# Kernel tuning notes

Hardware: AMD Instinct MI355X
Metric: run time of the kernel (lower is better)

The kernel has to match this reference:

```python
import jax, jax.numpy as jnp
import numpy as np

NUM_CP = 32

def setup_inputs() -> dict:
    key = jax.random.key(0)
    kx, kc = jax.random.split(key)
    x = jax.random.normal(kx, (64, 1048576), dtype=jnp.float32)
    control_points = jax.random.normal(kc, (NUM_CP,), dtype=jnp.float32) / np.sqrt(NUM_CP).astype(np.float32)
    knots = jnp.linspace(0.0, 1.0, NUM_CP, dtype=jnp.float32)
    return {"x": x, "control_points": control_points, "knots": knots}

def reference(x, control_points, knots):
    # normalize x to [0, ~1) exactly like the torch module
    xn = (x - x.min()) / (x.max() - x.min() + 1e-6)
    n = knots.shape[0]
    # bucketize: bin index i such that knots[i] <= xn < knots[i+1]
    # (points exactly on an interior knot give t=0 in the right bin, which equals
    idx = jnp.clip(jnp.searchsorted(knots, xn, side='right') - 1, 0, n - 2)
    k0 = knots[idx]
    k1 = knots[idx + 1]
    t = (xn - k0) / (k1 - k0)
    out = (1.0 - t) * control_points[idx] + t * control_points[idx + 1]
    # torch loop leaves points outside [knots[0], knots[-1]] at zero
    in_range = (xn >= knots[0]) & (xn <= knots[-1])
    return jnp.where(in_range, out, jnp.zeros((), dtype=out.dtype))
```

## Files before the change

### kernel.cpp

```cpp
#include <hip/hip_runtime.h>

typedef unsigned int u32;
typedef float vf4 __attribute__((ext_vector_type(4)));

__device__ __forceinline__ void nt_store4(float4* p, float4 v) {
    __builtin_nontemporal_store(*reinterpret_cast<vf4*>(&v), reinterpret_cast<vf4*>(p));
}
__device__ __forceinline__ float4 nt_load4(const float4* p) {
    vf4 t = __builtin_nontemporal_load(reinterpret_cast<const vf4*>(p));
    float4 r; r.x = t.x; r.y = t.y; r.z = t.z; r.w = t.w;
    return r;
}

__device__ __forceinline__ u32 f2ord(float f) {
    u32 b = __float_as_uint(f);
    return (b & 0x80000000u) ? ~b : (b | 0x80000000u);
}
__device__ __forceinline__ float ord2f(u32 k) {
    u32 b = (k & 0x80000000u) ? (k ^ 0x80000000u) : ~k;
    return __uint_as_float(b);
}

__global__ __launch_bounds__(256) void minmax_kernel(const float4* __restrict__ x, int n4,
                                                     u32* __restrict__ ws) {
    float mn = INFINITY, mx = -INFINITY;
    int stride = gridDim.x * blockDim.x;
    for (int i = blockIdx.x * blockDim.x + threadIdx.x; i < n4; i += stride) {
        float4 v = x[i];
        mn = fminf(mn, fminf(fminf(v.x, v.y), fminf(v.z, v.w)));
        mx = fmaxf(mx, fmaxf(fmaxf(v.x, v.y), fmaxf(v.z, v.w)));
    }
    #pragma unroll
    for (int off = 32; off > 0; off >>= 1) {
        mn = fminf(mn, __shfl_down(mn, off, 64));
        mx = fmaxf(mx, __shfl_down(mx, off, 64));
    }
    __shared__ float smn[4], smx[4];
    int wave = threadIdx.x >> 6;
    int lane = threadIdx.x & 63;
    if (lane == 0) { smn[wave] = mn; smx[wave] = mx; }
    __syncthreads();
    if (threadIdx.x == 0) {
        #pragma unroll
        for (int w = 1; w < 4; ++w) { mn = fminf(mn, smn[w]); mx = fmaxf(mx, smx[w]); }
        atomicMax(&ws[0], ~f2ord(mn));
        atomicMax(&ws[1],  f2ord(mx));
    }
}

__global__ __launch_bounds__(256) void apply_kernel(const float4* __restrict__ x,
                                                    const float* __restrict__ cp,
                                                    const float* __restrict__ knots,
                                                    const u32* __restrict__ ws,
                                                    float4* __restrict__ out, int n4) {
    __shared__ float sk[32];
    __shared__ float sa[32];
    __shared__ float sb[32];
    if (threadIdx.x < 32) {
        sk[threadIdx.x] = knots[threadIdx.x];
        sa[threadIdx.x] = cp[threadIdx.x];
    }
    __syncthreads();
    if (threadIdx.x < 31) {
        int i = threadIdx.x;
        sb[i] = (sa[i + 1] - sa[i]) / (sk[i + 1] - sk[i]);
    }
    __syncthreads();

    float mn = ord2f(~ws[0]);
    float mx = ord2f(ws[1]);
    float scale = 1.0f / (mx - mn + 1e-6f);
    float klo = sk[0], khi = sk[31];

    const int gtid   = blockIdx.x * blockDim.x + threadIdx.x;
    const int stride = gridDim.x * blockDim.x;
    const int KMAX   = (n4 + stride - 1) / stride;

    for (int k = KMAX - 1; k >= 0; --k) {
        const int i = k * stride + gtid;
        if (i >= n4) continue;
        float4 v = nt_load4(&x[i]);
        float4 r;
        float* vp = (float*)&v;
        float* rp = (float*)&r;
        #pragma unroll
        for (int c = 0; c < 4; ++c) {
            float xn = (vp[c] - mn) * scale;
            int b = (int)(xn * 31.0f);
            b = b < 0 ? 0 : (b > 30 ? 30 : b);
            if (xn < sk[b]) {
                b = (b > 0) ? b - 1 : 0;
            } else if (xn >= sk[b + 1]) {
                b = (b < 30) ? b + 1 : 30;
            }
            float val = fmaf(xn - sk[b], sb[b], sa[b]);
            rp[c] = (xn >= klo && xn <= khi) ? val : 0.0f;
        }
        nt_store4(&out[i], r);
    }
}

extern "C" void kernel_launch(void* const* d_in, const int* in_sizes, int n_in,
                              void* d_out, int out_size, void* d_ws, size_t ws_size,
                              hipStream_t stream) {
    const float* x     = (const float*)d_in[0];
    const float* cp    = (const float*)d_in[1];
    const float* knots = (const float*)d_in[2];
    float* out = (float*)d_out;
    u32* ws = (u32*)d_ws;

    int n  = in_sizes[0];
    int n4 = n / 4;

    hipMemsetAsync(ws, 0x00, 8, stream);

    minmax_kernel<<<4096, 256, 0, stream>>>((const float4*)x, n4, ws);
    apply_kernel <<<8192, 256, 0, stream>>>((const float4*)x, cp, knots, ws,
                                            (float4*)out, n4);
}
```

Baseline: 510.3 us.

## Fuse min/max reduction and spline apply into one cooperative kernel with grid sync

Merges the two kernels and the memset into a single cooperative launch. Each block writes its partial min/max to the workspace, a grid-wide sync follows, and then every block reduces all partials itself instead of using atomics. The apply phase walks the data in reverse order and handles two float4s per iteration, so the tail of the input may still be in cache from the first pass. This removes two launches and the atomic traffic, at the cost of a grid barrier and a fixed grid of 1024 blocks that must all be co-resident.

```diff
diff --git a/kernel.cpp b/kernel.cpp
--- a/kernel.cpp
+++ b/kernel.cpp
@@ -1,7 +1,12 @@
 #include <hip/hip_runtime.h>
+#include <hip/hip_cooperative_groups.h>
 
-typedef unsigned int u32;
+namespace cg = cooperative_groups;
+
 typedef float vf4 __attribute__((ext_vector_type(4)));
+
+#define NB 1024
+#define NT 256
 
 __device__ __forceinline__ void nt_store4(float4* p, float4 v) {
     __builtin_nontemporal_store(*reinterpret_cast<vf4*>(&v), reinterpret_cast<vf4*>(p));
@@ -12,50 +17,52 @@
     return r;
 }
 
-__device__ __forceinline__ u32 f2ord(float f) {
-    u32 b = __float_as_uint(f);
-    return (b & 0x80000000u) ? ~b : (b | 0x80000000u);
-}
-__device__ __forceinline__ float ord2f(u32 k) {
-    u32 b = (k & 0x80000000u) ? (k ^ 0x80000000u) : ~k;
-    return __uint_as_float(b);
-}
-
-__global__ __launch_bounds__(256) void minmax_kernel(const float4* __restrict__ x, int n4,
-                                                     u32* __restrict__ ws) {
-    float mn = INFINITY, mx = -INFINITY;
-    int stride = gridDim.x * blockDim.x;
-    for (int i = blockIdx.x * blockDim.x + threadIdx.x; i < n4; i += stride) {
-        float4 v = x[i];
-        mn = fminf(mn, fminf(fminf(v.x, v.y), fminf(v.z, v.w)));
-        mx = fmaxf(mx, fmaxf(fmaxf(v.x, v.y), fmaxf(v.z, v.w)));
-    }
+__device__ __forceinline__ void block_minmax(float& mn, float& mx,
+                                             volatile float* smn, volatile float* smx) {
     #pragma unroll
     for (int off = 32; off > 0; off >>= 1) {
         mn = fminf(mn, __shfl_down(mn, off, 64));
         mx = fmaxf(mx, __shfl_down(mx, off, 64));
     }
-    __shared__ float smn[4], smx[4];
     int wave = threadIdx.x >> 6;
     int lane = threadIdx.x & 63;
     if (lane == 0) { smn[wave] = mn; smx[wave] = mx; }
     __syncthreads();
     if (threadIdx.x == 0) {
         #pragma unroll
-        for (int w = 1; w < 4; ++w) { mn = fminf(mn, smn[w]); mx = fmaxf(mx, smx[w]); }
-        atomicMax(&ws[0], ~f2ord(mn));
-        atomicMax(&ws[1],  f2ord(mx));
+        for (int w = 1; w < NT / 64; ++w) {
+            mn = fminf(mn, smn[w]);
+            mx = fmaxf(mx, smx[w]);
+        }
     }
 }
 
-__global__ __launch_bounds__(256) void apply_kernel(const float4* __restrict__ x,
-                                                    const float* __restrict__ cp,
-                                                    const float* __restrict__ knots,
-                                                    const u32* __restrict__ ws,
-                                                    float4* __restrict__ out, int n4) {
+__device__ __forceinline__ float spline_eval(float xv, float mn, float scale,
+                                             const float* sk, const float* sa,
+                                             const float* sb, float klo, float khi) {
+    float xn = (xv - mn) * scale;
+    int b = (int)(xn * 31.0f);
+    b = b < 0 ? 0 : (b > 30 ? 30 : b);
+    if (xn < sk[b]) {
+        b = (b > 0) ? b - 1 : 0;
+    } else if (xn >= sk[b + 1]) {
+        b = (b < 30) ? b + 1 : 30;
+    }
+    float val = fmaf(xn - sk[b], sb[b], sa[b]);
+    return (xn >= klo && xn <= khi) ? val : 0.0f;
+}
+
+__global__ __launch_bounds__(NT, 4) void spline_fused(const float4* __restrict__ x,
+                                                      const float* __restrict__ cp,
+                                                      const float* __restrict__ knots,
+                                                      float* __restrict__ ws,
+                                                      float4* __restrict__ out, int n4) {
     __shared__ float sk[32];
     __shared__ float sa[32];
     __shared__ float sb[32];
+    __shared__ float smn[NT / 64], smx[NT / 64];
+    __shared__ float sbc[2];
+
     if (threadIdx.x < 32) {
         sk[threadIdx.x] = knots[threadIdx.x];
         sa[threadIdx.x] = cp[threadIdx.x];
@@ -65,56 +72,93 @@
         int i = threadIdx.x;
         sb[i] = (sa[i + 1] - sa[i]) / (sk[i + 1] - sk[i]);
     }
+
+    const int gtid   = blockIdx.x * NT + threadIdx.x;
+    const int stride = NB * NT;
+
+    float mn = INFINITY, mx = -INFINITY;
+    int i = gtid;
+    for (; i + stride < n4; i += 2 * stride) {
+        float4 a = x[i];
+        float4 b = x[i + stride];
+        mn = fminf(mn, fminf(fminf(a.x, a.y), fminf(a.z, a.w)));
+        mx = fmaxf(mx, fmaxf(fmaxf(a.x, a.y), fmaxf(a.z, a.w)));
+        mn = fminf(mn, fminf(fminf(b.x, b.y), fminf(b.z, b.w)));
+        mx = fmaxf(mx, fmaxf(fmaxf(b.x, b.y), fmaxf(b.z, b.w)));
+    }
+    for (; i < n4; i += stride) {
+        float4 a = x[i];
+        mn = fminf(mn, fminf(fminf(a.x, a.y), fminf(a.z, a.w)));
+        mx = fmaxf(mx, fmaxf(fmaxf(a.x, a.y), fmaxf(a.z, a.w)));
+    }
+    block_minmax(mn, mx, smn, smx);
+    if (threadIdx.x == 0) {
+        __hip_atomic_store(&ws[blockIdx.x],      mn, __ATOMIC_RELAXED, __HIP_MEMORY_SCOPE_AGENT);
+        __hip_atomic_store(&ws[NB + blockIdx.x], mx, __ATOMIC_RELAXED, __HIP_MEMORY_SCOPE_AGENT);
+        __threadfence();
+    }
+
+    cg::this_grid().sync();
+
+    mn = INFINITY; mx = -INFINITY;
+    for (int j = threadIdx.x; j < NB; j += NT) {
+        mn = fminf(mn, __hip_atomic_load(&ws[j],      __ATOMIC_RELAXED, __HIP_MEMORY_SCOPE_AGENT));
+        mx = fmaxf(mx, __hip_atomic_load(&ws[NB + j], __ATOMIC_RELAXED, __HIP_MEMORY_SCOPE_AGENT));
+    }
+    block_minmax(mn, mx, smn, smx);
+    if (threadIdx.x == 0) { sbc[0] = mn; sbc[1] = mx; }
     __syncthreads();
+    mn = sbc[0]; mx = sbc[1];
 
-    float mn = ord2f(~ws[0]);
-    float mx = ord2f(ws[1]);
-    float scale = 1.0f / (mx - mn + 1e-6f);
-    float klo = sk[0], khi = sk[31];
+    const float scale = 1.0f / (mx - mn + 1e-6f);
+    const float klo = sk[0], khi = sk[31];
 
-    const int gtid   = blockIdx.x * blockDim.x + threadIdx.x;
-    const int stride = gridDim.x * blockDim.x;
-    const int KMAX   = (n4 + stride - 1) / stride;
-
-    for (int k = KMAX - 1; k >= 0; --k) {
-        const int i = k * stride + gtid;
-        if (i >= n4) continue;
-        float4 v = nt_load4(&x[i]);
-        float4 r;
-        float* vp = (float*)&v;
-        float* rp = (float*)&r;
-        #pragma unroll
-        for (int c = 0; c < 4; ++c) {
-            float xn = (vp[c] - mn) * scale;
-            int b = (int)(xn * 31.0f);
-            b = b < 0 ? 0 : (b > 30 ? 30 : b);
-            if (xn < sk[b]) {
-                b = (b > 0) ? b - 1 : 0;
-            } else if (xn >= sk[b + 1]) {
-                b = (b < 30) ? b + 1 : 30;
-            }
-            float val = fmaf(xn - sk[b], sb[b], sa[b]);
-            rp[c] = (xn >= klo && xn <= khi) ? val : 0.0f;
+    const int KMAX = (n4 + stride - 1) / stride;
+    int k = KMAX - 1;
+    for (; k >= 1; k -= 2) {
+        const int i0 = k * stride + gtid;
+        const int i1 = (k - 1) * stride + gtid;
+        const bool ok0 = (i0 < n4);
+        float4 v0 = ok0 ? nt_load4(&x[i0]) : make_float4(0.f, 0.f, 0.f, 0.f);
+        float4 v1 = nt_load4(&x[i1]);
+        float4 r0, r1;
+        r0.x = spline_eval(v0.x, mn, scale, sk, sa, sb, klo, khi);
+        r0.y = spline_eval(v0.y, mn, scale, sk, sa, sb, klo, khi);
+        r0.z = spline_eval(v0.z, mn, scale, sk, sa, sb, klo, khi);
+        r0.w = spline_eval(v0.w, mn, scale, sk, sa, sb, klo, khi);
+        r1.x = spline_eval(v1.x, mn, scale, sk, sa, sb, klo, khi);
+        r1.y = spline_eval(v1.y, mn, scale, sk, sa, sb, klo, khi);
+        r1.z = spline_eval(v1.z, mn, scale, sk, sa, sb, klo, khi);
+        r1.w = spline_eval(v1.w, mn, scale, sk, sa, sb, klo, khi);
+        if (ok0) nt_store4(&out[i0], r0);
+        nt_store4(&out[i1], r1);
+    }
+    if (k == 0) {
+        const int i0 = gtid;
+        if (i0 < n4) {
+            float4 v0 = nt_load4(&x[i0]);
+            float4 r0;
+            r0.x = spline_eval(v0.x, mn, scale, sk, sa, sb, klo, khi);
+            r0.y = spline_eval(v0.y, mn, scale, sk, sa, sb, klo, khi);
+            r0.z = spline_eval(v0.z, mn, scale, sk, sa, sb, klo, khi);
+            r0.w = spline_eval(v0.w, mn, scale, sk, sa, sb, klo, khi);
+            nt_store4(&out[i0], r0);
         }
-        nt_store4(&out[i], r);
     }
 }
 
 extern "C" void kernel_launch(void* const* d_in, const int* in_sizes, int n_in,
                               void* d_out, int out_size, void* d_ws, size_t ws_size,
                               hipStream_t stream) {
-    const float* x     = (const float*)d_in[0];
-    const float* cp    = (const float*)d_in[1];
-    const float* knots = (const float*)d_in[2];
-    float* out = (float*)d_out;
-    u32* ws = (u32*)d_ws;
+    const float4* x     = (const float4*)d_in[0];
+    const float*  cp    = (const float*)d_in[1];
+    const float*  knots = (const float*)d_in[2];
+    float*  ws  = (float*)d_ws;
+    float4* out = (float4*)d_out;
 
     int n  = in_sizes[0];
     int n4 = n / 4;
 
-    hipMemsetAsync(ws, 0x00, 8, stream);
-
-    minmax_kernel<<<4096, 256, 0, stream>>>((const float4*)x, n4, ws);
-    apply_kernel <<<8192, 256, 0, stream>>>((const float4*)x, cp, knots, ws,
-                                            (float4*)out, n4);
+    void* args[] = {(void*)&x, (void*)&cp, (void*)&knots, (void*)&ws, (void*)&out, (void*)&n4};
+    hipLaunchCooperativeKernel((const void*)spline_fused, dim3(NB), dim3(NT), args, 0, stream);
 }
```

After: 636.5 us. 24.7% more time.
